# Optimization experiments

Measured on AMD Instinct MI355X. Metric: run time of the kernel, lower is better.

The kernel has to match this reference:

```python
import jax, jax.numpy as jnp
import numpy as np

D_MODEL = 1024
N_HEADS = 16
D_HEAD = D_MODEL // N_HEADS
B, S = 4, 2048


def setup_inputs() -> dict:
    key = jax.random.key(0)
    ks = jax.random.split(key, 8)
    scale = 1.0 / np.sqrt(D_MODEL)
    x = jax.random.normal(ks[0], (B, S, D_MODEL), dtype=jnp.float32)
    relative_bias = jax.random.normal(ks[1], (1, N_HEADS, S, S), dtype=jnp.float32)
    w_q = jax.random.normal(ks[2], (D_MODEL, D_MODEL), dtype=jnp.float32) * scale
    w_k = jax.random.normal(ks[3], (D_MODEL, D_MODEL), dtype=jnp.float32) * scale
    w_v = jax.random.normal(ks[4], (D_MODEL, D_MODEL), dtype=jnp.float32) * scale
    w_o = jax.random.normal(ks[5], (D_MODEL, D_MODEL), dtype=jnp.float32) * scale
    b_o = jax.random.normal(ks[6], (D_MODEL,), dtype=jnp.float32) * 0.02
    return {"x": x, "relative_bias": relative_bias, "w_q": w_q, "w_k": w_k,
            "w_v": w_v, "w_o": w_o, "b_o": b_o}


def reference(x, relative_bias, w_q, w_k, w_v, w_o, b_o):
    b, s, d = x.shape
    # torch nn.Linear computes x @ W^T; weights stored [out, in]
    def proj(w):
        y = jnp.einsum('bsd,ed->bse', x, w)  # [B,S,D]
        return y.reshape(b, s, N_HEADS, D_HEAD).transpose(0, 2, 1, 3)  # [B,H,S,Dh]
    q, k, v = proj(w_q), proj(w_k), proj(w_v)
    scores = jnp.einsum('bhqd,bhkd->bhqk', q, k) / jnp.sqrt(
        jnp.asarray(D_HEAD, x.dtype)) + relative_bias
    attn = jax.nn.softmax(scores, axis=-1)
    ctx = jnp.einsum('bhqk,bhkd->bhqd', attn, v)
    ctx = ctx.transpose(0, 2, 1, 3).reshape(b, s, d)
    return jnp.einsum('bsd,ed->bse', ctx, w_o) + b_o
```

## Files before the change

### kernel.cpp

```cpp
#include <hip/hip_runtime.h>
#include <hip/hip_bf16.h>

#define D_MODEL 1024
#define N_HEADS 16
#define D_HEAD  64
#define BATCH   4
#define SEQ     2048

typedef __attribute__((ext_vector_type(8))) short short8;
typedef __attribute__((ext_vector_type(8))) unsigned short ushort8;
typedef __attribute__((ext_vector_type(4))) unsigned short ushort4v;
typedef __attribute__((ext_vector_type(4))) float f32x4;

__device__ inline unsigned short f2bf(float f) {
  unsigned int u = __builtin_bit_cast(unsigned int, f);
  u += 0x7fffu + ((u >> 16) & 1u);
  return (unsigned short)(u >> 16);
}

__device__ inline f32x4 mfma_bf16(short8 a, short8 b, f32x4 c) {
  return __builtin_amdgcn_mfma_f32_16x16x32_bf16(a, b, c, 0, 0, 0);
}

__global__ void cvt_kernel(const float* __restrict__ src,
                           unsigned short* __restrict__ dst, int n) {
  int i = (blockIdx.x * 256 + threadIdx.x) * 8;
  if (i >= n) return;
  float4 a = *reinterpret_cast<const float4*>(src + i);
  float4 b = *reinterpret_cast<const float4*>(src + i + 4);
  ushort8 o;
  o[0] = f2bf(a.x); o[1] = f2bf(a.y); o[2] = f2bf(a.z); o[3] = f2bf(a.w);
  o[4] = f2bf(b.x); o[5] = f2bf(b.y); o[6] = f2bf(b.z); o[7] = f2bf(b.w);
  *reinterpret_cast<ushort8*>(dst + i) = o;
}

template<int NBYTES>
__device__ inline void stage_swz(const unsigned short* g0, int g_stride_elems,
                                 unsigned short* lds0, int tid) {
#pragma unroll
  for (int it = 0; it < NBYTES / 4096; ++it) {
    int o = it * 4096 + tid * 16;
    int r = o >> 7;
    int cb = (o & 127) ^ ((r & 7) << 4);
    unsigned short* g = const_cast<unsigned short*>(g0) +
                        (size_t)r * g_stride_elems + (cb >> 1);
    unsigned short* l = lds0 + (o >> 1);
    __builtin_amdgcn_global_load_lds((__attribute__((address_space(1))) void*)g,
                                     (__attribute__((address_space(3))) void*)l,
                                     16, 0, 0);
  }
}

__device__ inline short8 frag_ld(const unsigned short* tile, int row, int col_el) {
  int cb = (col_el << 1) ^ ((row & 7) << 4);
  return *reinterpret_cast<const short8*>(
      reinterpret_cast<const char*>(tile) + row * 128 + cb);
}

__launch_bounds__(256, 2)
__global__ void qkv_gemm(const unsigned short* __restrict__ xb,
                         const unsigned short* __restrict__ wb,
                         unsigned short* __restrict__ Qo,
                         unsigned short* __restrict__ Ko,
                         unsigned short* __restrict__ Vt) {
  __shared__ __align__(16) unsigned short As[128][64];
  __shared__ __align__(16) unsigned short Bs[128][64];
  const int z = blockIdx.z;
  const int m0 = blockIdx.y * 128;
  const int n0 = blockIdx.x * 128;
  const int tid = threadIdx.x;
  const int lane = tid & 63;
  const int wv = tid >> 6;
  const int wr = wv >> 1, wc = wv & 1;
  const int lrow = lane & 15;
  const int lk8 = (lane >> 4) << 3;
  const unsigned short* w = wb + (size_t)z * D_MODEL * D_MODEL;

  f32x4 acc[4][4];
  const f32x4 zero = {0.f, 0.f, 0.f, 0.f};
#pragma unroll
  for (int i = 0; i < 4; ++i)
#pragma unroll
    for (int j = 0; j < 4; ++j) acc[i][j] = zero;

  for (int k0 = 0; k0 < D_MODEL; k0 += 64) {
    __syncthreads();
    stage_swz<16384>(xb + (size_t)m0 * D_MODEL + k0, D_MODEL, &As[0][0], tid);
    stage_swz<16384>(w  + (size_t)n0 * D_MODEL + k0, D_MODEL, &Bs[0][0], tid);
    __syncthreads();
#pragma unroll
    for (int ks = 0; ks < 2; ++ks) {
      short8 af[4], bfr[4];
#pragma unroll
      for (int mi = 0; mi < 4; ++mi)
        af[mi] = frag_ld(&As[0][0], wr * 64 + mi * 16 + lrow, ks * 32 + lk8);
#pragma unroll
      for (int ni = 0; ni < 4; ++ni)
        bfr[ni] = frag_ld(&Bs[0][0], wc * 64 + ni * 16 + lrow, ks * 32 + lk8);
      if (z != 2) {
#pragma unroll
        for (int mi = 0; mi < 4; ++mi)
#pragma unroll
          for (int ni = 0; ni < 4; ++ni)
            acc[mi][ni] = mfma_bf16(af[mi], bfr[ni], acc[mi][ni]);
      } else {
#pragma unroll
        for (int ni = 0; ni < 4; ++ni)
#pragma unroll
          for (int mi = 0; mi < 4; ++mi)
            acc[ni][mi] = mfma_bf16(bfr[ni], af[mi], acc[ni][mi]);
      }
    }
  }

  const int lrr = (lane >> 4) << 2;
  if (z != 2) {
    unsigned short* dst = (z == 0) ? Qo : Ko;
    const float scale = (z == 0) ? 0.125f : 1.0f;
#pragma unroll
    for (int mi = 0; mi < 4; ++mi)
#pragma unroll
      for (int ni = 0; ni < 4; ++ni)
#pragma unroll
        for (int r = 0; r < 4; ++r) {
          int m = m0 + wr * 64 + mi * 16 + lrr + r;
          int e = n0 + wc * 64 + ni * 16 + lrow;
          int b = m >> 11, s = m & (SEQ - 1);
          int h = e >> 6, dh = e & 63;
          dst[((size_t)(b * N_HEADS + h) * SEQ + s) * D_HEAD + dh] =
              f2bf(acc[mi][ni][r] * scale);
        }
  } else {
#pragma unroll
    for (int ni = 0; ni < 4; ++ni)
#pragma unroll
      for (int mi = 0; mi < 4; ++mi)
#pragma unroll
        for (int r = 0; r < 4; ++r) {
          int e = n0 + wc * 64 + ni * 16 + lrr + r;
          int m = m0 + wr * 64 + mi * 16 + lrow;
          int b = m >> 11, s = m & (SEQ - 1);
          int h = e >> 6, dh = e & 63;
          Vt[((size_t)(b * N_HEADS + h) * D_HEAD + dh) * SEQ + s] =
              f2bf(acc[ni][mi][r]);
        }
  }
}

__launch_bounds__(256, 2)
__global__ void attn_kernel(const unsigned short* __restrict__ Q,
                            const unsigned short* __restrict__ K,
                            const unsigned short* __restrict__ Vt,
                            const float* __restrict__ bias,
                            unsigned short* __restrict__ ctx) {
  __shared__ __align__(16) unsigned short Qs[64][64];
  __shared__ __align__(16) unsigned short Ks[2][64][64];
  __shared__ __align__(16) unsigned short Vs[2][64][64];
  __shared__ __align__(16) unsigned short Ps[4][16][72];

  const int fid = blockIdx.y * 32 + blockIdx.x;
  const int j = fid >> 3;
  const int h = (fid & 7) + 8 * (j & 1);
  const int q0 = (j >> 1) * 64;

  const int tid = threadIdx.x, lane = tid & 63, wv = tid >> 6;
  const int lrow = lane & 15;
  const int lgrp = lane >> 4;
  const int lk8 = lgrp << 3;
  const int lrr = lgrp << 2;

  short8 qf[4][2];
#pragma unroll
  for (int b = 0; b < 4; ++b) {
    stage_swz<8192>(Q + ((size_t)(b * N_HEADS + h) * SEQ + q0) * D_HEAD,
                    D_HEAD, &Qs[0][0], tid);
    __syncthreads();
#pragma unroll
    for (int ks = 0; ks < 2; ++ks)
      qf[b][ks] = frag_ld(&Qs[0][0], wv * 16 + lrow, ks * 32 + lk8);
    __syncthreads();
  }

  stage_swz<8192>(K + (size_t)h * SEQ * D_HEAD, D_HEAD, &Ks[0][0][0], tid);
  stage_swz<8192>(Vt + (size_t)h * D_HEAD * SEQ, SEQ, &Vs[0][0][0], tid);

  const float* bp = bias + (size_t)h * SEQ * SEQ +
                    (size_t)(q0 + wv * 16 + lrow) * SEQ + lrr;
  f32x4 bcur[4], bnext[4];
#pragma unroll
  for (int nt = 0; nt < 4; ++nt)
    bcur[nt] = __builtin_nontemporal_load(
        reinterpret_cast<const f32x4*>(bp + nt * 16));

  float m_run[4], l_run[4];
  f32x4 o_acc[4][4];
  const f32x4 zero = {0.f, 0.f, 0.f, 0.f};
#pragma unroll
  for (int b = 0; b < 4; ++b) {
    m_run[b] = -1e30f; l_run[b] = 0.f;
#pragma unroll
    for (int dt = 0; dt < 4; ++dt) o_acc[b][dt] = zero;
  }

  __syncthreads();

  for (int kt = 0; kt < 32; ++kt) {
    if (kt < 31) {
#pragma unroll
      for (int nt = 0; nt < 4; ++nt)
        bnext[nt] = __builtin_nontemporal_load(
            reinterpret_cast<const f32x4*>(bp + (kt + 1) * 64 + nt * 16));
    }

#pragma unroll
    for (int b = 0; b < 4; ++b) {
      const int cur = b & 1;

      if (!(kt == 31 && b == 3)) {
        const int nb = (b + 1) & 3;
        const int nkt = kt + (b == 3 ? 1 : 0);
        stage_swz<8192>(K + (size_t)(nb * N_HEADS + h) * SEQ * D_HEAD +
                            (size_t)nkt * 64 * D_HEAD,
                        D_HEAD, &Ks[cur ^ 1][0][0], tid);
        stage_swz<8192>(Vt + (size_t)(nb * N_HEADS + h) * D_HEAD * SEQ +
                            nkt * 64,
                        SEQ, &Vs[cur ^ 1][0][0], tid);
      }

      f32x4 s[4];
#pragma unroll
      for (int nt = 0; nt < 4; ++nt) s[nt] = zero;
      __builtin_amdgcn_s_setprio(1);
#pragma unroll
      for (int ks = 0; ks < 2; ++ks)
#pragma unroll
        for (int nt = 0; nt < 4; ++nt) {
          short8 kf = frag_ld(&Ks[cur][0][0], nt * 16 + lrow, ks * 32 + lk8);
          s[nt] = mfma_bf16(kf, qf[b][ks], s[nt]);
        }
      __builtin_amdgcn_s_setprio(0);

      float p[4][4];
      float pmax = -1e30f;
#pragma unroll
      for (int nt = 0; nt < 4; ++nt)
#pragma unroll
        for (int r = 0; r < 4; ++r) {
          float v = s[nt][r] + bcur[nt][r];
          p[nt][r] = v;
          pmax = fmaxf(pmax, v);
        }
      pmax = fmaxf(pmax, __shfl_xor(pmax, 16));
      pmax = fmaxf(pmax, __shfl_xor(pmax, 32));
      float mnew = fmaxf(m_run[b], pmax);
      float corr = __expf(m_run[b] - mnew);
      float rs = 0.f;
#pragma unroll
      for (int nt = 0; nt < 4; ++nt)
#pragma unroll
        for (int r = 0; r < 4; ++r) {
          float e = __expf(p[nt][r] - mnew);
          p[nt][r] = e;
          rs += e;
        }
      rs += __shfl_xor(rs, 16);
      rs += __shfl_xor(rs, 32);
      l_run[b] = l_run[b] * corr + rs;
      m_run[b] = mnew;

#pragma unroll
      for (int nt = 0; nt < 4; ++nt) {
        ushort4v pk;
#pragma unroll
        for (int r = 0; r < 4; ++r) pk[r] = f2bf(p[nt][r]);
        *reinterpret_cast<ushort4v*>(&Ps[wv][lrow][nt * 16 + lrr]) = pk;
      }

#pragma unroll
      for (int r = 0; r < 4; ++r) {
        float c = __shfl(corr, lrr + r);
#pragma unroll
        for (int dt = 0; dt < 4; ++dt) o_acc[b][dt][r] *= c;
      }

      short8 pf[2];
#pragma unroll
      for (int ks = 0; ks < 2; ++ks)
        pf[ks] = *reinterpret_cast<const short8*>(&Ps[wv][lrow][ks * 32 + lk8]);
      __builtin_amdgcn_s_setprio(1);
#pragma unroll
      for (int ks = 0; ks < 2; ++ks)
#pragma unroll
        for (int dt = 0; dt < 4; ++dt) {
          short8 vf = frag_ld(&Vs[cur][0][0], dt * 16 + lrow, ks * 32 + lk8);
          o_acc[b][dt] = mfma_bf16(pf[ks], vf, o_acc[b][dt]);
        }
      __builtin_amdgcn_s_setprio(0);

      __syncthreads();
    }

    if (kt < 31) {
#pragma unroll
      for (int nt = 0; nt < 4; ++nt) bcur[nt] = bnext[nt];
    }
  }

#pragma unroll
  for (int b = 0; b < 4; ++b) {
    float inv = 1.0f / l_run[b];
#pragma unroll
    for (int r = 0; r < 4; ++r) {
      float invq = __shfl(inv, lrr + r);
      int qs = q0 + wv * 16 + lrr + r;
#pragma unroll
      for (int dt = 0; dt < 4; ++dt)
        ctx[((size_t)b * SEQ + qs) * D_MODEL + h * 64 + dt * 16 + lrow] =
            f2bf(o_acc[b][dt][r] * invq);
    }
  }
}

__launch_bounds__(256, 2)
__global__ void out_gemm(const unsigned short* __restrict__ cb,
                         const unsigned short* __restrict__ wo,
                         const float* __restrict__ bo,
                         float* __restrict__ out) {
  __shared__ __align__(16) unsigned short As[128][64];
  __shared__ __align__(16) unsigned short Bs[128][64];
  const int m0 = blockIdx.y * 128;
  const int n0 = blockIdx.x * 128;
  const int tid = threadIdx.x;
  const int lane = tid & 63;
  const int wv = tid >> 6;
  const int wr = wv >> 1, wc = wv & 1;
  const int lrow = lane & 15;
  const int lk8 = (lane >> 4) << 3;

  f32x4 acc[4][4];
  const f32x4 zero = {0.f, 0.f, 0.f, 0.f};
#pragma unroll
  for (int i = 0; i < 4; ++i)
#pragma unroll
    for (int j = 0; j < 4; ++j) acc[i][j] = zero;

  for (int k0 = 0; k0 < D_MODEL; k0 += 64) {
    __syncthreads();
    stage_swz<16384>(cb + (size_t)m0 * D_MODEL + k0, D_MODEL, &As[0][0], tid);
    stage_swz<16384>(wo + (size_t)n0 * D_MODEL + k0, D_MODEL, &Bs[0][0], tid);
    __syncthreads();
#pragma unroll
    for (int ks = 0; ks < 2; ++ks) {
      short8 af[4], bfr[4];
#pragma unroll
      for (int mi = 0; mi < 4; ++mi)
        af[mi] = frag_ld(&As[0][0], wr * 64 + mi * 16 + lrow, ks * 32 + lk8);
#pragma unroll
      for (int ni = 0; ni < 4; ++ni)
        bfr[ni] = frag_ld(&Bs[0][0], wc * 64 + ni * 16 + lrow, ks * 32 + lk8);
#pragma unroll
      for (int mi = 0; mi < 4; ++mi)
#pragma unroll
        for (int ni = 0; ni < 4; ++ni)
          acc[mi][ni] = mfma_bf16(af[mi], bfr[ni], acc[mi][ni]);
    }
  }

  const int lrr = (lane >> 4) << 2;
#pragma unroll
  for (int mi = 0; mi < 4; ++mi)
#pragma unroll
    for (int ni = 0; ni < 4; ++ni)
#pragma unroll
      for (int r = 0; r < 4; ++r) {
        int m = m0 + wr * 64 + mi * 16 + lrr + r;
        int e = n0 + wc * 64 + ni * 16 + lrow;
        out[(size_t)m * D_MODEL + e] = acc[mi][ni][r] + bo[e];
      }
}

extern "C" void kernel_launch(void* const* d_in, const int* in_sizes, int n_in,
                              void* d_out, int out_size, void* d_ws, size_t ws_size,
                              hipStream_t stream) {
  const float* x    = (const float*)d_in[0];
  const float* bias = (const float*)d_in[1];
  const float* w_q  = (const float*)d_in[2];
  const float* w_k  = (const float*)d_in[3];
  const float* w_v  = (const float*)d_in[4];
  const float* w_o  = (const float*)d_in[5];
  const float* b_o  = (const float*)d_in[6];
  float* out = (float*)d_out;

  const size_t NX = (size_t)BATCH * SEQ * D_MODEL;
  const size_t NW = (size_t)D_MODEL * D_MODEL;

  unsigned short* xb    = (unsigned short*)d_ws;
  unsigned short* wqkvb = xb + NX;
  unsigned short* wob   = wqkvb + 3 * NW;
  unsigned short* Qb    = wob + NW;
  unsigned short* Kb    = Qb + NX;
  unsigned short* Vtb   = Kb + NX;
  unsigned short* ctxb  = Vtb + NX;

  cvt_kernel<<<(int)(NX / 2048), 256, 0, stream>>>(x, xb, (int)NX);
  cvt_kernel<<<(int)(NW / 2048), 256, 0, stream>>>(w_q, wqkvb, (int)NW);
  cvt_kernel<<<(int)(NW / 2048), 256, 0, stream>>>(w_k, wqkvb + NW, (int)NW);
  cvt_kernel<<<(int)(NW / 2048), 256, 0, stream>>>(w_v, wqkvb + 2 * NW, (int)NW);
  cvt_kernel<<<(int)(NW / 2048), 256, 0, stream>>>(w_o, wob, (int)NW);

  qkv_gemm<<<dim3(8, 64, 3), 256, 0, stream>>>(xb, wqkvb, Qb, Kb, Vtb);
  attn_kernel<<<dim3(32, 16), 256, 0, stream>>>(Qb, Kb, Vtb, bias, ctxb);
  out_gemm<<<dim3(8, 64), 256, 0, stream>>>(ctxb, wob, b_o, out);
}
```

Baseline: 305.1 us.

## Split attention batches across two blocks, use exp2 softmax with lazy rescaling

The attention grid doubles so that each block handles two batches instead of four, with launch bounds raised to three blocks per CU. This raises occupancy, but each bias tile is now read by two blocks instead of one. Q is pre-scaled by log2e and the bias is folded into the MFMA accumulator init, so the softmax can use the native exp2 instruction. The online-softmax rescale is skipped while the running max grows by at most 11 in log2 space. Bias loads switch from nontemporal to normal loads, and the bf16 conversion now uses the library intrinsic.

```diff
diff --git a/kernel.cpp b/kernel.cpp
--- a/kernel.cpp
+++ b/kernel.cpp
@@ -6,6 +6,7 @@
 #define D_HEAD  64
 #define BATCH   4
 #define SEQ     2048
+#define LOG2E   1.44269504088896f
 
 typedef __attribute__((ext_vector_type(8))) short short8;
 typedef __attribute__((ext_vector_type(8))) unsigned short ushort8;
@@ -16,6 +17,10 @@
   unsigned int u = __builtin_bit_cast(unsigned int, f);
   u += 0x7fffu + ((u >> 16) & 1u);
   return (unsigned short)(u >> 16);
+}
+
+__device__ inline float exp2_fast(float x) {
+  return __builtin_amdgcn_exp2f(x);
 }
 
 __device__ inline f32x4 mfma_bf16(short8 a, short8 b, f32x4 c) {
@@ -116,7 +121,7 @@
   const int lrr = (lane >> 4) << 2;
   if (z != 2) {
     unsigned short* dst = (z == 0) ? Qo : Ko;
-    const float scale = (z == 0) ? 0.125f : 1.0f;
+    const float scale = (z == 0) ? 0.125f * LOG2E : 1.0f;
 #pragma unroll
     for (int mi = 0; mi < 4; ++mi)
 #pragma unroll
@@ -147,7 +152,7 @@
   }
 }
 
-__launch_bounds__(256, 2)
+__launch_bounds__(256, 3)
 __global__ void attn_kernel(const unsigned short* __restrict__ Q,
                             const unsigned short* __restrict__ K,
                             const unsigned short* __restrict__ Vt,
@@ -158,10 +163,11 @@
   __shared__ __align__(16) unsigned short Vs[2][64][64];
   __shared__ __align__(16) unsigned short Ps[4][16][72];
 
-  const int fid = blockIdx.y * 32 + blockIdx.x;
-  const int j = fid >> 3;
-  const int h = (fid & 7) + 8 * (j & 1);
-  const int q0 = (j >> 1) * 64;
+  const int lid = blockIdx.x + 32 * blockIdx.y + 512 * blockIdx.z;
+  const int xg = lid & 7, g = lid >> 3;
+  const int bg = g & 1;
+  const int h = (xg << 1) | ((g >> 1) & 1);
+  const int q0 = ((g >> 2) & 31) << 6;
 
   const int tid = threadIdx.x, lane = tid & 63, wv = tid >> 6;
   const int lrow = lane & 15;
@@ -169,10 +175,11 @@
   const int lk8 = lgrp << 3;
   const int lrr = lgrp << 2;
 
-  short8 qf[4][2];
-#pragma unroll
-  for (int b = 0; b < 4; ++b) {
-    stage_swz<8192>(Q + ((size_t)(b * N_HEADS + h) * SEQ + q0) * D_HEAD,
+  short8 qf[2][2];
+#pragma unroll
+  for (int b = 0; b < 2; ++b) {
+    const int bb = bg * 2 + b;
+    stage_swz<8192>(Q + ((size_t)(bb * N_HEADS + h) * SEQ + q0) * D_HEAD,
                     D_HEAD, &Qs[0][0], tid);
     __syncthreads();
 #pragma unroll
@@ -181,22 +188,23 @@
     __syncthreads();
   }
 
-  stage_swz<8192>(K + (size_t)h * SEQ * D_HEAD, D_HEAD, &Ks[0][0][0], tid);
-  stage_swz<8192>(Vt + (size_t)h * D_HEAD * SEQ, SEQ, &Vs[0][0][0], tid);
+  stage_swz<8192>(K + (size_t)(bg * 2 * N_HEADS + h) * SEQ * D_HEAD, D_HEAD,
+                  &Ks[0][0][0], tid);
+  stage_swz<8192>(Vt + (size_t)(bg * 2 * N_HEADS + h) * D_HEAD * SEQ, SEQ,
+                  &Vs[0][0][0], tid);
 
   const float* bp = bias + (size_t)h * SEQ * SEQ +
                     (size_t)(q0 + wv * 16 + lrow) * SEQ + lrr;
   f32x4 bcur[4], bnext[4];
 #pragma unroll
   for (int nt = 0; nt < 4; ++nt)
-    bcur[nt] = __builtin_nontemporal_load(
-        reinterpret_cast<const f32x4*>(bp + nt * 16));
-
-  float m_run[4], l_run[4];
-  f32x4 o_acc[4][4];
+    bcur[nt] = *reinterpret_cast<const f32x4*>(bp + nt * 16) * LOG2E;
+
+  float m_run[2], l_run[2];
+  f32x4 o_acc[2][4];
   const f32x4 zero = {0.f, 0.f, 0.f, 0.f};
 #pragma unroll
-  for (int b = 0; b < 4; ++b) {
+  for (int b = 0; b < 2; ++b) {
     m_run[b] = -1e30f; l_run[b] = 0.f;
 #pragma unroll
     for (int dt = 0; dt < 4; ++dt) o_acc[b][dt] = zero;
@@ -208,17 +216,17 @@
     if (kt < 31) {
 #pragma unroll
       for (int nt = 0; nt < 4; ++nt)
-        bnext[nt] = __builtin_nontemporal_load(
-            reinterpret_cast<const f32x4*>(bp + (kt + 1) * 64 + nt * 16));
-    }
-
-#pragma unroll
-    for (int b = 0; b < 4; ++b) {
-      const int cur = b & 1;
-
-      if (!(kt == 31 && b == 3)) {
-        const int nb = (b + 1) & 3;
-        const int nkt = kt + (b == 3 ? 1 : 0);
+        bnext[nt] = *reinterpret_cast<const f32x4*>(bp + (kt + 1) * 64 +
+                                                    nt * 16) * LOG2E;
+    }
+
+#pragma unroll
+    for (int b = 0; b < 2; ++b) {
+      const int cur = b;
+
+      if (!(kt == 31 && b == 1)) {
+        const int nb = bg * 2 + (b ^ 1);
+        const int nkt = kt + b;
         stage_swz<8192>(K + (size_t)(nb * N_HEADS + h) * SEQ * D_HEAD +
                             (size_t)nkt * 64 * D_HEAD,
                         D_HEAD, &Ks[cur ^ 1][0][0], tid);
@@ -229,7 +237,7 @@
 
       f32x4 s[4];
 #pragma unroll
-      for (int nt = 0; nt < 4; ++nt) s[nt] = zero;
+      for (int nt = 0; nt < 4; ++nt) s[nt] = bcur[nt];
       __builtin_amdgcn_s_setprio(1);
 #pragma unroll
       for (int ks = 0; ks < 2; ++ks)
@@ -240,47 +248,51 @@
         }
       __builtin_amdgcn_s_setprio(0);
 
-      float p[4][4];
-      float pmax = -1e30f;
-#pragma unroll
-      for (int nt = 0; nt < 4; ++nt)
-#pragma unroll
-        for (int r = 0; r < 4; ++r) {
-          float v = s[nt][r] + bcur[nt][r];
-          p[nt][r] = v;
-          pmax = fmaxf(pmax, v);
-        }
+      float pmax =
+          fmaxf(fmaxf(fmaxf(fmaxf(s[0][0], s[0][1]), s[0][2]),
+                      fmaxf(fmaxf(s[1][0], s[1][1]), s[1][2])),
+                fmaxf(fmaxf(fmaxf(s[2][0], s[2][1]), s[2][2]),
+                      fmaxf(fmaxf(fmaxf(s[3][0], s[3][1]), s[3][2]),
+                            fmaxf(fmaxf(s[0][3], s[1][3]),
+                                  fmaxf(s[2][3], s[3][3])))));
       pmax = fmaxf(pmax, __shfl_xor(pmax, 16));
       pmax = fmaxf(pmax, __shfl_xor(pmax, 32));
-      float mnew = fmaxf(m_run[b], pmax);
-      float corr = __expf(m_run[b] - mnew);
+
+      if (!__all(pmax - m_run[b] <= 11.0f)) {
+        float mnew = fmaxf(m_run[b], pmax);
+        float corr = exp2_fast(m_run[b] - mnew);
+        l_run[b] *= corr;
+        m_run[b] = mnew;
+#pragma unroll
+        for (int r = 0; r < 4; ++r) {
+          float c = __shfl(corr, lrr + r);
+#pragma unroll
+          for (int dt = 0; dt < 4; ++dt) o_acc[b][dt][r] *= c;
+        }
+      }
+
+      float p[4][4];
       float rs = 0.f;
 #pragma unroll
       for (int nt = 0; nt < 4; ++nt)
 #pragma unroll
         for (int r = 0; r < 4; ++r) {
-          float e = __expf(p[nt][r] - mnew);
+          float e = exp2_fast(s[nt][r] - m_run[b]);
           p[nt][r] = e;
           rs += e;
         }
       rs += __shfl_xor(rs, 16);
       rs += __shfl_xor(rs, 32);
-      l_run[b] = l_run[b] * corr + rs;
-      m_run[b] = mnew;
+      l_run[b] += rs;
 
 #pragma unroll
       for (int nt = 0; nt < 4; ++nt) {
         ushort4v pk;
 #pragma unroll
-        for (int r = 0; r < 4; ++r) pk[r] = f2bf(p[nt][r]);
+        for (int r = 0; r < 4; ++r)
+          pk[r] = __builtin_bit_cast(unsigned short,
+                                     __float2bfloat16(p[nt][r]));
         *reinterpret_cast<ushort4v*>(&Ps[wv][lrow][nt * 16 + lrr]) = pk;
-      }
-
-#pragma unroll
-      for (int r = 0; r < 4; ++r) {
-        float c = __shfl(corr, lrr + r);
-#pragma unroll
-        for (int dt = 0; dt < 4; ++dt) o_acc[b][dt][r] *= c;
       }
 
       short8 pf[2];
@@ -307,7 +319,8 @@
   }
 
 #pragma unroll
-  for (int b = 0; b < 4; ++b) {
+  for (int b = 0; b < 2; ++b) {
+    const int bb = bg * 2 + b;
     float inv = 1.0f / l_run[b];
 #pragma unroll
     for (int r = 0; r < 4; ++r) {
@@ -315,7 +328,7 @@
       int qs = q0 + wv * 16 + lrr + r;
 #pragma unroll
       for (int dt = 0; dt < 4; ++dt)
-        ctx[((size_t)b * SEQ + qs) * D_MODEL + h * 64 + dt * 16 + lrow] =
+        ctx[((size_t)bb * SEQ + qs) * D_MODEL + h * 64 + dt * 16 + lrow] =
             f2bf(o_acc[b][dt][r] * invq);
     }
   }
@@ -409,6 +422,6 @@
   cvt_kernel<<<(int)(NW / 2048), 256, 0, stream>>>(w_o, wob, (int)NW);
 
   qkv_gemm<<<dim3(8, 64, 3), 256, 0, stream>>>(xb, wqkvb, Qb, Kb, Vtb);
-  attn_kernel<<<dim3(32, 16), 256, 0, stream>>>(Qb, Kb, Vtb, bias, ctxb);
+  attn_kernel<<<dim3(32, 16, 2), 256, 0, stream>>>(Qb, Kb, Vtb, bias, ctxb);
   out_gemm<<<dim3(8, 64), 256, 0, stream>>>(ctxb, wob, b_o, out);
 }
```

After: 322.4 us. 5.7% more time.
